# Kernel tuning notes

Hardware: AMD Instinct MI355X
Metric: run time of the kernel (lower is better)

Reference implementation:

```python
import jax, jax.numpy as jnp
import numpy as np

K_F = 3
NUM = K_F * K_F - 1          # 8 non-center neighbors
IDX_REF = NUM // 2           # 4 (center insertion index)
PROP_TIME = 18
AFFINITY_GAMMA = 0.5
B, H, W = 4, 480, 640


def _bilinear(img, y, x):
    """Bilinear sample img [H,W] at float coords y,x [K,H,W]; zero outside."""
    Hh, Ww = img.shape
    y0 = jnp.floor(y)
    x0 = jnp.floor(x)

    def gather(yy, xx):
        valid = (yy >= 0) & (yy < Hh) & (xx >= 0) & (xx < Ww)
        yi = jnp.clip(yy.astype(jnp.int32), 0, Hh - 1)
        xi = jnp.clip(xx.astype(jnp.int32), 0, Ww - 1)
        return jnp.where(valid, img[yi, xi], 0.0)

    wy = y - y0
    wx = x - x0
    return ((1 - wy) * (1 - wx) * gather(y0, x0)
            + (1 - wy) * wx * gather(y0, x0 + 1)
            + wy * (1 - wx) * gather(y0 + 1, x0)
            + wy * wx * gather(y0 + 1, x0 + 1))


def _deform_prop(feat, dy, dx, aff):
    """Modulated deformable 3x3 conv with all-ones weight, zero bias, ch=1.
    feat [B,1,H,W]; dy,dx,aff [B,9,H,W]. Output = sum_k aff_k * sample_k."""
    b, _, h, w = feat.shape
    ky = jnp.array([-1, -1, -1, 0, 0, 0, 1, 1, 1], feat.dtype)
    kx = jnp.array([-1, 0, 1, -1, 0, 1, -1, 0, 1], feat.dtype)
    gy = jnp.arange(h, dtype=feat.dtype)[:, None]   # [H,1]
    gx = jnp.arange(w, dtype=feat.dtype)[None, :]   # [1,W]
    py = gy[None, None] + ky[None, :, None, None] + dy  # [B,9,H,W]
    px = gx[None, None] + kx[None, :, None, None] + dx
    samp = jax.vmap(_bilinear)(feat[:, 0], py, px)      # [B,9,H,W]
    return jnp.sum(samp * aff, axis=1, keepdims=True)


def _affinity_normalization(aff, scale):
    # TGASS: tanh / (gamma*num), abs-sum normalize (clamped at 1), reference = 1 - sum
    aff = jnp.tanh(aff) / (scale + 1e-8)
    s = jnp.sum(jnp.abs(aff), axis=1, keepdims=True) + 1e-4
    s = jnp.maximum(s, 1.0)
    aff = aff / s
    aff_ref = 1.0 - jnp.sum(aff, axis=1, keepdims=True)
    return jnp.concatenate([aff[:, :IDX_REF], aff_ref, aff[:, IDX_REF:]], axis=1)


def setup_inputs() -> dict:
    key = jax.random.key(0)
    k1, k2, k3, k4, k5 = jax.random.split(key, 5)
    feat_init = jax.random.uniform(k1, (B, 1, H, W), jnp.float32) * 10.0
    guidance = jax.random.normal(k2, (B, 24, H, W), jnp.float32)
    confidence = jax.random.uniform(k3, (B, 1, H, W), jnp.float32)
    dense = jax.random.uniform(k4, (B, 1, H, W), jnp.float32) * 10.0
    mask = (jax.random.uniform(k5, (B, 1, H, W)) < 0.05).astype(jnp.float32)
    feat_fix = dense * mask
    aff_scale_const = jnp.full((1,), AFFINITY_GAMMA * NUM, jnp.float32)
    return {"feat_init": feat_init, "guidance": guidance,
            "confidence": confidence, "feat_fix": feat_fix,
            "aff_scale_const": aff_scale_const}


def reference(feat_init, guidance, confidence, feat_fix, aff_scale_const):
    b = feat_init.shape[0]
    h, w = feat_init.shape[2], feat_init.shape[3]
    # offsets: chunk guidance into (o1, o2, aff), interleave, insert zero at center
    o1, o2, aff_g = jnp.split(guidance, 3, axis=1)
    off = jnp.concatenate([o1, o2], axis=1).reshape(b, NUM, 2, h, w)
    zc = jnp.zeros((b, 1, 2, h, w), off.dtype)
    off = jnp.concatenate([off[:, :IDX_REF], zc, off[:, IDX_REF:]], axis=1)
    dy, dx = off[:, :, 0], off[:, :, 1]          # [B,9,H,W]
    aff = _affinity_normalization(aff_g, aff_scale_const)

    # preserve_input: fixed-pixel mask (ch_f == 1)
    mask_fix = (feat_fix > 0.0).astype(feat_init.dtype)
    conf = (1.0 - mask_fix) * confidence + mask_fix
    feat = (1.0 - mask_fix) * feat_init + mask_fix * feat_fix

    def step(f, _):
        f = _deform_prop(f * conf, dy, dx, aff)
        f = (1.0 - mask_fix) * f + mask_fix * feat_fix
        return f, None

    feat, _ = jax.lax.scan(step, feat, None, length=PROP_TIME)
    return feat
```

## Files before the change

### kernel.cpp

```cpp
#include <hip/hip_runtime.h>
#include <hip/hip_fp16.h>


#define HH 480
#define WW 640
#define BB 4
#define HWSZ (HH * WW)
#define NPIX (BB * HWSZ)
#define PROP_T 18
#define SLACK 704
#define NTHR 256
#define PXT 10
#define NBLK (NPIX / (NTHR * PXT))

#define TOUCH1(v)  asm volatile("" : "+v"(v))
#define TOUCH4(v)  do { TOUCH1((v).x); TOUCH1((v).y); TOUCH1((v).z); TOUCH1((v).w); } while (0)

struct f2u { float x, y; };

__device__ __forceinline__ float fast_tanh(float x) {
    x = fminf(fmaxf(x, -15.0f), 15.0f);
    float e = __expf(2.0f * x);
    return __fdividef(e - 1.0f, e + 1.0f);
}

__device__ __forceinline__ float affinities(const float* gb, float inv_scale,
                                            float t[8]) {
    float ssum = 1e-4f;
#pragma unroll
    for (int j = 0; j < 8; ++j) {
        float v = fast_tanh(gb[(16 + j) * HWSZ]) * inv_scale;
        t[j] = v; ssum += fabsf(v);
    }
    ssum = fmaxf(ssum, 1.0f);
    float rs = __fdividef(1.0f, ssum);
    float asum = 0.0f;
#pragma unroll
    for (int j = 0; j < 8; ++j) { t[j] *= rs; asum += t[j]; }
    return 1.0f - asum;
}

__device__ __forceinline__ void make_desc(int y, int x, int k,
                                          float dy, float dx, float ak,
                                          unsigned& pk, unsigned short& akh) {
    float py = (float)(y + k / 3 - 1) + dy;
    float px = (float)(x + k % 3 - 1) + dx;
    float y0f = floorf(py), x0f = floorf(px);
    float wy = py - y0f, wx = px - x0f;
    int y0 = (int)y0f, x0 = (int)x0f;
    if (y0 == -1)                 { ak *= wy;        wy = 1.0f; }
    else if (y0 == HH - 1)        { ak *= 1.0f - wy; wy = 0.0f; }
    else if (y0 < -1 || y0 >= HH) { ak = 0.0f; }
    if (x0 == -1)                 { ak *= wx;        wx = 1.0f; }
    else if (x0 == WW - 1)        { ak *= 1.0f - wx; wx = 0.0f; }
    else if (x0 < -1 || x0 >= WW) { ak = 0.0f; }
    int rel;
    if (ak == 0.0f) {
        rel = 0; wy = 0.0f; wx = 0.0f;
    } else {
        int yc = min(max(y0, -1), HH - 1);
        int xc = min(max(x0, -1), WW - 1);
        rel = (yc - y) * WW + (xc - x);
        rel = min(max(rel, -32767), 32767);
    }
    unsigned uy = (unsigned)(int)(wy * 255.0f + 0.5f);
    unsigned ux = (unsigned)(int)(wx * 255.0f + 0.5f);
    pk  = ((unsigned)(unsigned short)(short)rel << 16) | (uy << 8) | ux;
    akh = __half_as_ushort(__float2half(ak));
}

__device__ __forceinline__ float sample_rel(const float* __restrict__ fp,
                                            unsigned pk, unsigned short akh,
                                            float acc) {
    int rel = (int)(short)(pk >> 16);
    float wy = (float)((pk >> 8) & 0xffu) * (1.0f / 255.0f);
    float wx = (float)(pk & 0xffu) * (1.0f / 255.0f);
    float ak = __half2float(__ushort_as_half(akh));
    const float* p = fp + rel;
    f2u r0 = *reinterpret_cast<const f2u*>(p);
    f2u r1 = *reinterpret_cast<const f2u*>(p + WW);
    float bot = ak * wy;
    float top = ak - bot;
    float omwx = 1.0f - wx;
    acc = fmaf(top * omwx, r0.x, acc);
    acc = fmaf(top * wx,   r0.y, acc);
    acc = fmaf(bot * omwx, r1.x, acc);
    acc = fmaf(bot * wx,   r1.y, acc);
    return acc;
}

__device__ __forceinline__ void gsync(unsigned* __restrict__ bar,
                                      unsigned target) {
    __threadfence();
    __syncthreads();
    if (threadIdx.x == 0) {
        atomicAdd(bar, 1u);
        while (__hip_atomic_load(bar, __ATOMIC_ACQUIRE,
                                 __HIP_MEMORY_SCOPE_AGENT) < target) {
            __builtin_amdgcn_s_sleep(2);
        }
    }
    __syncthreads();
    __threadfence();
}

__global__ __launch_bounds__(NTHR) void precompute_kernel(
    const float* __restrict__ feat_init,
    const float* __restrict__ guid,
    const float* __restrict__ confidence,
    const float* __restrict__ feat_fix,
    const float* __restrict__ aff_scale,
    float* __restrict__ g0,
    unsigned* __restrict__ pk1Arr,
    unsigned short* __restrict__ akArr,
    uint2* __restrict__ cffpArr) {
    const int pix = blockIdx.x * NTHR + threadIdx.x;
    const int b = pix / HWSZ;
    const int q = pix - b * HWSZ;
    const int y = q / WW;
    const int x = q - y * WW;
    const float* gb = guid + (size_t)b * 24 * HWSZ + q;

    float ff = feat_fix[pix];
    float m  = (ff > 0.0f) ? 1.0f : 0.0f;
    float km = 1.0f - m;
    float conf = km * confidence[pix] + m;
    float f0   = km * feat_init[pix] + m * ff;
    g0[pix] = f0 * conf;

    const float inv_scale = __fdividef(1.0f, aff_scale[0] + 1e-8f);
    float t[8];
    float aref = affinities(gb, inv_scale, t);
    unsigned cf = ((unsigned)__half_as_ushort(__float2half(aref)) << 16)
                | (unsigned)__half_as_ushort(__float2half(conf));
    cffpArr[pix] = make_uint2(cf, __float_as_uint(m * ff));

    unsigned pk[8];
    unsigned short akh[8];
#pragma unroll
    for (int n = 0; n < 8; ++n) {
        const int k = (n < 4) ? n : (n + 1);
        float dy = gb[(2 * n) * HWSZ];
        float dx = gb[(2 * n + 1) * HWSZ];
        make_desc(y, x, k, dy, dx, t[n], pk[n], akh[n]);
    }
    uint4* pd = reinterpret_cast<uint4*>(pk1Arr) + 2 * pix;
    pd[0] = make_uint4(pk[0], pk[1], pk[2], pk[3]);
    pd[1] = make_uint4(pk[4], pk[5], pk[6], pk[7]);
    uint4 kv;
    kv.x = (unsigned)akh[0] | ((unsigned)akh[1] << 16);
    kv.y = (unsigned)akh[2] | ((unsigned)akh[3] << 16);
    kv.z = (unsigned)akh[4] | ((unsigned)akh[5] << 16);
    kv.w = (unsigned)akh[6] | ((unsigned)akh[7] << 16);
    reinterpret_cast<uint4*>(akArr)[pix] = kv;
}

__global__ __launch_bounds__(NTHR, 2) void persist_kernel(
    const unsigned* __restrict__ pk1Arr,
    const unsigned short* __restrict__ akArr,
    const uint2* __restrict__ cffpArr,
    float* __restrict__ fA,
    float* __restrict__ fB,
    float* __restrict__ out,
    unsigned* __restrict__ bar)
{
    const int base = blockIdx.x * (NTHR * PXT) + threadIdx.x;

    uint4 pka[PXT], pkb[PXT], akv[PXT];
    unsigned cfx[PXT];
    float    ffv[PXT];

#pragma unroll
    for (int i = 0; i < PXT; ++i) {
        const int pix = base + i * NTHR;
        const uint4* pd = reinterpret_cast<const uint4*>(pk1Arr) + 2 * pix;
        pka[i] = pd[0];
        pkb[i] = pd[1];
        akv[i] = reinterpret_cast<const uint4*>(akArr)[pix];
        uint2 cw = cffpArr[pix];
        cfx[i] = cw.x;
        ffv[i] = __uint_as_float(cw.y);
    }
#pragma unroll
    for (int i = 0; i < PXT; ++i) {
        TOUCH4(pka[i]); TOUCH4(pkb[i]); TOUCH4(akv[i]);
        TOUCH1(cfx[i]); TOUCH1(ffv[i]);
    }

#pragma unroll 1
    for (int t = 0; t < PROP_T; ++t) {
        if (t) gsync(bar, (unsigned)NBLK * (unsigned)t);
        const float* fin = (t & 1) ? fB : fA;
        float* fout = (t == PROP_T - 1) ? out : ((t & 1) ? fA : fB);
        const bool last = (t == PROP_T - 1);
#pragma unroll
        for (int i = 0; i < PXT; ++i) {
            const int pix = base + i * NTHR;
            const float* fp = fin + pix;
            float aref = __half2float(__ushort_as_half((unsigned short)(cfx[i] >> 16)));
            float conf = __half2float(__ushort_as_half((unsigned short)(cfx[i] & 0xffffu)));
            float acc = aref * fp[0];
            uint4 A = pka[i], B = pkb[i], K = akv[i];
            acc = sample_rel(fp, A.x, (unsigned short)(K.x & 0xffffu), acc);
            acc = sample_rel(fp, A.y, (unsigned short)(K.x >> 16),     acc);
            acc = sample_rel(fp, A.z, (unsigned short)(K.y & 0xffffu), acc);
            acc = sample_rel(fp, A.w, (unsigned short)(K.y >> 16),     acc);
            acc = sample_rel(fp, B.x, (unsigned short)(K.z & 0xffffu), acc);
            acc = sample_rel(fp, B.y, (unsigned short)(K.z >> 16),     acc);
            acc = sample_rel(fp, B.z, (unsigned short)(K.w & 0xffffu), acc);
            acc = sample_rel(fp, B.w, (unsigned short)(K.w >> 16),     acc);
            float km = (ffv[i] > 0.0f) ? 0.0f : 1.0f;
            float fnew = fmaf(km, acc, ffv[i]);
            fout[pix] = last ? fnew : conf * fnew;
        }
    }
}

__global__ __launch_bounds__(NTHR) void step_kernel(
    const float* __restrict__ fin,
    float* __restrict__ fout,
    const unsigned* __restrict__ pk1Arr,
    const unsigned short* __restrict__ akArr,
    const uint2* __restrict__ cffpArr,
    int last) {
    const int pix = blockIdx.x * NTHR + threadIdx.x;
    const float* fp = fin + pix;
    const uint4* pd = reinterpret_cast<const uint4*>(pk1Arr) + 2 * pix;
    uint4 A = pd[0], B = pd[1];
    uint4 K = reinterpret_cast<const uint4*>(akArr)[pix];
    uint2 cw = cffpArr[pix];
    float ffv = __uint_as_float(cw.y);
    float aref = __half2float(__ushort_as_half((unsigned short)(cw.x >> 16)));
    float conf = __half2float(__ushort_as_half((unsigned short)(cw.x & 0xffffu)));
    float acc = aref * fp[0];
    acc = sample_rel(fp, A.x, (unsigned short)(K.x & 0xffffu), acc);
    acc = sample_rel(fp, A.y, (unsigned short)(K.x >> 16),     acc);
    acc = sample_rel(fp, A.z, (unsigned short)(K.y & 0xffffu), acc);
    acc = sample_rel(fp, A.w, (unsigned short)(K.y >> 16),     acc);
    acc = sample_rel(fp, B.x, (unsigned short)(K.z & 0xffffu), acc);
    acc = sample_rel(fp, B.y, (unsigned short)(K.z >> 16),     acc);
    acc = sample_rel(fp, B.z, (unsigned short)(K.w & 0xffffu), acc);
    acc = sample_rel(fp, B.w, (unsigned short)(K.w >> 16),     acc);
    float km = (ffv > 0.0f) ? 0.0f : 1.0f;
    float fnew = fmaf(km, acc, ffv);
    fout[pix] = last ? fnew : conf * fnew;
}

extern "C" void kernel_launch(void* const* d_in, const int* in_sizes, int n_in,
                              void* d_out, int out_size, void* d_ws, size_t ws_size,
                              hipStream_t stream) {
    const float* feat_init  = (const float*)d_in[0];
    const float* guidance   = (const float*)d_in[1];
    const float* confidence = (const float*)d_in[2];
    const float* feat_fix   = (const float*)d_in[3];
    const float* aff_scale  = (const float*)d_in[4];

    const size_t bufFloats = (size_t)NPIX + 2 * SLACK;
    float* bufA = (float*)d_ws;
    float* bufB = bufA + bufFloats;
    unsigned* pk1Arr = (unsigned*)(bufB + bufFloats);
    unsigned short* akArr = (unsigned short*)(pk1Arr + 8 * (size_t)NPIX);
    uint2* cffpArr = (uint2*)(akArr + 8 * (size_t)NPIX);
    unsigned* bar = (unsigned*)(cffpArr + NPIX);
    float* fA = bufA + SLACK;
    float* fB = bufB + SLACK;
    float* outp = (float*)d_out;

    hipMemsetAsync(bufA, 0, SLACK * sizeof(float), stream);
    hipMemsetAsync(bufA + SLACK + NPIX, 0, SLACK * sizeof(float), stream);
    hipMemsetAsync(bufB, 0, SLACK * sizeof(float), stream);
    hipMemsetAsync(bufB + SLACK + NPIX, 0, SLACK * sizeof(float), stream);
    hipMemsetAsync(bar, 0, 16, stream);

    precompute_kernel<<<NPIX / NTHR, NTHR, 0, stream>>>(
        feat_init, guidance, confidence, feat_fix, aff_scale,
        fA, pk1Arr, akArr, cffpArr);

    bool tryPersist = false;
    {
        int occ = 0;
        if (hipOccupancyMaxActiveBlocksPerMultiprocessor(
                &occ, reinterpret_cast<const void*>(persist_kernel), NTHR, 0)
                == hipSuccess) {
            int dev = 0, cu = 0;
            hipGetDevice(&dev);
            hipDeviceGetAttribute(&cu, hipDeviceAttributeMultiprocessorCount, dev);
            if ((long)occ * cu >= NBLK) tryPersist = true;
        }
    }
    if (tryPersist) {
        persist_kernel<<<NBLK, NTHR, 0, stream>>>(
            pk1Arr, akArr, cffpArr, fA, fB, outp, bar);
        return;
    }

    for (int t = 0; t < PROP_T; ++t) {
        const float* fin = (t & 1) ? fB : fA;
        float* fout = (t == PROP_T - 1) ? outp : ((t & 1) ? fA : fB);
        step_kernel<<<NPIX / NTHR, NTHR, 0, stream>>>(
            fin, fout, pk1Arr, akArr, cffpArr, (t == PROP_T - 1) ? 1 : 0);
    }
}
```

Baseline: 655.9 us.

## Move most per-pixel sample descriptors from registers into LDS in persistent kernel

The persistent kernel previously kept all eight packed sample descriptors per pixel in VGPRs across the 18 propagation steps. Seven of them now live in shared memory, loaded once before the step loop and re-read from LDS each step, while one descriptor plus the affinities, confidence and fixed values stay in registers. The launch-bounds hint for two blocks per CU is also dropped. This lowers register pressure, which may avoid spills, but adds LDS reads on every step and uses about 70 KB of LDS per block. That LDS size may cap occupancy or fail if the grid assumes a set number of co-resident blocks for the grid barrier.

```diff
diff --git a/kernel.cpp b/kernel.cpp
--- a/kernel.cpp
+++ b/kernel.cpp
@@ -155,7 +155,7 @@
     reinterpret_cast<uint4*>(akArr)[pix] = kv;
 }
 
-__global__ __launch_bounds__(NTHR, 2) void persist_kernel(
+__global__ __launch_bounds__(NTHR) void persist_kernel(
     const unsigned* __restrict__ pk1Arr,
     const unsigned short* __restrict__ akArr,
     const uint2* __restrict__ cffpArr,
@@ -164,28 +164,39 @@
     float* __restrict__ out,
     unsigned* __restrict__ bar)
 {
+    __shared__ uint2    lds_p01[NTHR * PXT];
+    __shared__ uint2    lds_p23[NTHR * PXT];
+    __shared__ uint2    lds_p45[NTHR * PXT];
+    __shared__ unsigned lds_p6 [NTHR * PXT];
+
     const int base = blockIdx.x * (NTHR * PXT) + threadIdx.x;
 
-    uint4 pka[PXT], pkb[PXT], akv[PXT];
+    unsigned pk7r[PXT];
+    uint4    akv[PXT];
     unsigned cfx[PXT];
     float    ffv[PXT];
 
 #pragma unroll
     for (int i = 0; i < PXT; ++i) {
         const int pix = base + i * NTHR;
+        const int loc = i * NTHR + threadIdx.x;
         const uint4* pd = reinterpret_cast<const uint4*>(pk1Arr) + 2 * pix;
-        pka[i] = pd[0];
-        pkb[i] = pd[1];
-        akv[i] = reinterpret_cast<const uint4*>(akArr)[pix];
+        uint4 A = pd[0], Bv = pd[1];
+        lds_p01[loc] = make_uint2(A.x, A.y);
+        lds_p23[loc] = make_uint2(A.z, A.w);
+        lds_p45[loc] = make_uint2(Bv.x, Bv.y);
+        lds_p6 [loc] = Bv.z;
+        pk7r[i] = Bv.w;
+        akv[i]  = reinterpret_cast<const uint4*>(akArr)[pix];
         uint2 cw = cffpArr[pix];
         cfx[i] = cw.x;
         ffv[i] = __uint_as_float(cw.y);
     }
 #pragma unroll
     for (int i = 0; i < PXT; ++i) {
-        TOUCH4(pka[i]); TOUCH4(pkb[i]); TOUCH4(akv[i]);
-        TOUCH1(cfx[i]); TOUCH1(ffv[i]);
-    }
+        TOUCH1(pk7r[i]); TOUCH4(akv[i]); TOUCH1(cfx[i]); TOUCH1(ffv[i]);
+    }
+    __syncthreads();
 
 #pragma unroll 1
     for (int t = 0; t < PROP_T; ++t) {
@@ -196,19 +207,24 @@
 #pragma unroll
         for (int i = 0; i < PXT; ++i) {
             const int pix = base + i * NTHR;
+            const int loc = i * NTHR + threadIdx.x;
             const float* fp = fin + pix;
+            uint2 q01 = lds_p01[loc];
+            uint2 q23 = lds_p23[loc];
+            uint2 q45 = lds_p45[loc];
+            unsigned q6 = lds_p6[loc];
             float aref = __half2float(__ushort_as_half((unsigned short)(cfx[i] >> 16)));
             float conf = __half2float(__ushort_as_half((unsigned short)(cfx[i] & 0xffffu)));
             float acc = aref * fp[0];
-            uint4 A = pka[i], B = pkb[i], K = akv[i];
-            acc = sample_rel(fp, A.x, (unsigned short)(K.x & 0xffffu), acc);
-            acc = sample_rel(fp, A.y, (unsigned short)(K.x >> 16),     acc);
-            acc = sample_rel(fp, A.z, (unsigned short)(K.y & 0xffffu), acc);
-            acc = sample_rel(fp, A.w, (unsigned short)(K.y >> 16),     acc);
-            acc = sample_rel(fp, B.x, (unsigned short)(K.z & 0xffffu), acc);
-            acc = sample_rel(fp, B.y, (unsigned short)(K.z >> 16),     acc);
-            acc = sample_rel(fp, B.z, (unsigned short)(K.w & 0xffffu), acc);
-            acc = sample_rel(fp, B.w, (unsigned short)(K.w >> 16),     acc);
+            uint4 K = akv[i];
+            acc = sample_rel(fp, q01.x,   (unsigned short)(K.x & 0xffffu), acc);
+            acc = sample_rel(fp, q01.y,   (unsigned short)(K.x >> 16),     acc);
+            acc = sample_rel(fp, q23.x,   (unsigned short)(K.y & 0xffffu), acc);
+            acc = sample_rel(fp, q23.y,   (unsigned short)(K.y >> 16),     acc);
+            acc = sample_rel(fp, q45.x,   (unsigned short)(K.z & 0xffffu), acc);
+            acc = sample_rel(fp, q45.y,   (unsigned short)(K.z >> 16),     acc);
+            acc = sample_rel(fp, q6,      (unsigned short)(K.w & 0xffffu), acc);
+            acc = sample_rel(fp, pk7r[i], (unsigned short)(K.w >> 16),     acc);
             float km = (ffv[i] > 0.0f) ? 0.0f : 1.0f;
             float fnew = fmaf(km, acc, ffv[i]);
             fout[pix] = last ? fnew : conf * fnew;
```

Measured after the change: 658.0 us. No clear change (+0.3%).

## Stage feature rows plus halo in LDS per step in persistent kernel

Applied to the files above, without the earlier changes.

Each persistent block now copies its feature rows plus a six-row halo on each side into shared memory at every propagation step, and serves bilinear taps from LDS, falling back to global memory when an offset leaves the tile. Pixels per thread drop from 10 to 5, so the grid doubles, and the two-blocks-per-CU launch bound is removed. SLACK grows so the halo reads stay inside allocated buffers. The aim is to replace scattered global/L2 gathers with LDS reads. In exchange each step pays an extra tile copy and a __syncthreads, the grid-wide barrier has more blocks to wait on, and the 14-row tile (about 35 KB) limits occupancy.

```diff
diff --git a/kernel.cpp b/kernel.cpp
--- a/kernel.cpp
+++ b/kernel.cpp
@@ -8,10 +8,15 @@
 #define HWSZ (HH * WW)
 #define NPIX (BB * HWSZ)
 #define PROP_T 18
-#define SLACK 704
+#define SLACK 4096
 #define NTHR 256
-#define PXT 10
+#define PXT 5
 #define NBLK (NPIX / (NTHR * PXT))
+
+#define TILE_ROWS 14
+#define TILE_F (TILE_ROWS * WW)
+#define TILE_HALO (6 * WW)
+#define TILE_MAXOFF (TILE_F - WW - 2)
 
 #define TOUCH1(v)  asm volatile("" : "+v"(v))
 #define TOUCH4(v)  do { TOUCH1((v).x); TOUCH1((v).y); TOUCH1((v).z); TOUCH1((v).w); } while (0)
@@ -89,6 +94,35 @@
     return acc;
 }
 
+__device__ __forceinline__ float sample_tile(const float* tile,
+                                             const float* __restrict__ fp,
+                                             int off_base,
+                                             unsigned pk, unsigned short akh,
+                                             float acc) {
+    int rel = (int)(short)(pk >> 16);
+    float wy = (float)((pk >> 8) & 0xffu) * (1.0f / 255.0f);
+    float wx = (float)(pk & 0xffu) * (1.0f / 255.0f);
+    float ak = __half2float(__ushort_as_half(akh));
+    int off = off_base + rel;
+    f2u r0, r1;
+    if (off >= 0 && off <= TILE_MAXOFF) {
+        r0 = *reinterpret_cast<const f2u*>(tile + off);
+        r1 = *reinterpret_cast<const f2u*>(tile + off + WW);
+    } else {
+        const float* p = fp + rel;
+        r0 = *reinterpret_cast<const f2u*>(p);
+        r1 = *reinterpret_cast<const f2u*>(p + WW);
+    }
+    float bot = ak * wy;
+    float top = ak - bot;
+    float omwx = 1.0f - wx;
+    acc = fmaf(top * omwx, r0.x, acc);
+    acc = fmaf(top * wx,   r0.y, acc);
+    acc = fmaf(bot * omwx, r1.x, acc);
+    acc = fmaf(bot * wx,   r1.y, acc);
+    return acc;
+}
+
 __device__ __forceinline__ void gsync(unsigned* __restrict__ bar,
                                       unsigned target) {
     __threadfence();
@@ -155,7 +189,7 @@
     reinterpret_cast<uint4*>(akArr)[pix] = kv;
 }
 
-__global__ __launch_bounds__(NTHR, 2) void persist_kernel(
+__global__ __launch_bounds__(NTHR) void persist_kernel(
     const unsigned* __restrict__ pk1Arr,
     const unsigned short* __restrict__ akArr,
     const uint2* __restrict__ cffpArr,
@@ -164,7 +198,11 @@
     float* __restrict__ out,
     unsigned* __restrict__ bar)
 {
-    const int base = blockIdx.x * (NTHR * PXT) + threadIdx.x;
+    __shared__ float tile[TILE_F];
+
+    const int tid = threadIdx.x;
+    const int base = blockIdx.x * (NTHR * PXT);
+    const int lo = base - TILE_HALO;
 
     uint4 pka[PXT], pkb[PXT], akv[PXT];
     unsigned cfx[PXT];
@@ -172,7 +210,7 @@
 
 #pragma unroll
     for (int i = 0; i < PXT; ++i) {
-        const int pix = base + i * NTHR;
+        const int pix = base + i * NTHR + tid;
         const uint4* pd = reinterpret_cast<const uint4*>(pk1Arr) + 2 * pix;
         pka[i] = pd[0];
         pkb[i] = pd[1];
@@ -193,22 +231,34 @@
         const float* fin = (t & 1) ? fB : fA;
         float* fout = (t == PROP_T - 1) ? out : ((t & 1) ? fA : fB);
         const bool last = (t == PROP_T - 1);
+
+        const float4* src = reinterpret_cast<const float4*>(fin + lo);
+        float4* dst = reinterpret_cast<float4*>(tile);
+#pragma unroll
+        for (int j = 0; j < (TILE_F / 4 + NTHR - 1) / NTHR; ++j) {
+            int idx = j * NTHR + tid;
+            if (idx < TILE_F / 4) dst[idx] = src[idx];
+        }
+        __syncthreads();
+
 #pragma unroll
         for (int i = 0; i < PXT; ++i) {
-            const int pix = base + i * NTHR;
+            const int pl = i * NTHR + tid;
+            const int pix = base + pl;
+            const int ob = pl + TILE_HALO;
             const float* fp = fin + pix;
             float aref = __half2float(__ushort_as_half((unsigned short)(cfx[i] >> 16)));
             float conf = __half2float(__ushort_as_half((unsigned short)(cfx[i] & 0xffffu)));
-            float acc = aref * fp[0];
+            float acc = aref * tile[ob];
             uint4 A = pka[i], B = pkb[i], K = akv[i];
-            acc = sample_rel(fp, A.x, (unsigned short)(K.x & 0xffffu), acc);
-            acc = sample_rel(fp, A.y, (unsigned short)(K.x >> 16),     acc);
-            acc = sample_rel(fp, A.z, (unsigned short)(K.y & 0xffffu), acc);
-            acc = sample_rel(fp, A.w, (unsigned short)(K.y >> 16),     acc);
-            acc = sample_rel(fp, B.x, (unsigned short)(K.z & 0xffffu), acc);
-            acc = sample_rel(fp, B.y, (unsigned short)(K.z >> 16),     acc);
-            acc = sample_rel(fp, B.z, (unsigned short)(K.w & 0xffffu), acc);
-            acc = sample_rel(fp, B.w, (unsigned short)(K.w >> 16),     acc);
+            acc = sample_tile(tile, fp, ob, A.x, (unsigned short)(K.x & 0xffffu), acc);
+            acc = sample_tile(tile, fp, ob, A.y, (unsigned short)(K.x >> 16),     acc);
+            acc = sample_tile(tile, fp, ob, A.z, (unsigned short)(K.y & 0xffffu), acc);
+            acc = sample_tile(tile, fp, ob, A.w, (unsigned short)(K.y >> 16),     acc);
+            acc = sample_tile(tile, fp, ob, B.x, (unsigned short)(K.z & 0xffffu), acc);
+            acc = sample_tile(tile, fp, ob, B.y, (unsigned short)(K.z >> 16),     acc);
+            acc = sample_tile(tile, fp, ob, B.z, (unsigned short)(K.w & 0xffffu), acc);
+            acc = sample_tile(tile, fp, ob, B.w, (unsigned short)(K.w >> 16),     acc);
             float km = (ffv[i] > 0.0f) ? 0.0f : 1.0f;
             float fnew = fmaf(km, acc, ffv[i]);
             fout[pix] = last ? fnew : conf * fnew;
```

Measured after the change: 653.6 us. Within noise of the previous version (-0.3%).
